# Performance work log

Measured on AMD Instinct MI355X. Metric: run time of the kernel, lower is better.

## Reference

```python
import jax, jax.numpy as jnp
import numpy as np

N_NODES = 100000
N_EDGES = 3200000


def gcn_conv(x, src, dst, W, b, n):
    # PyG GCNConv: add self-loops, symmetric normalization, scatter-add to dst.
    loops = jnp.arange(n)
    s = jnp.concatenate([src, loops])
    d = jnp.concatenate([dst, loops])
    h = x @ W                                   # [N, out]
    deg = jnp.zeros((n,), h.dtype).at[d].add(1.0)
    dinv = jnp.where(deg > 0, jax.lax.rsqrt(deg), 0.0)
    norm = dinv[s] * dinv[d]                    # [E+N]
    msg = h[s] * norm[:, None]                  # gather + scale
    out = jax.ops.segment_sum(msg, d, num_segments=n)
    return out + b


def setup_inputs() -> dict:
    key = jax.random.key(0)
    ks = jax.random.split(key, 10)
    x1 = jax.random.normal(ks[0], (N_NODES, 3), dtype=jnp.float32)
    edge_index1 = jax.random.randint(ks[1], (2, N_EDGES), 0, N_NODES, dtype=jnp.int64 if jax.config.jax_enable_x64 else jnp.int32)
    def lin(k, fi, fo):
        s = 1.0 / np.sqrt(fi)
        kw, kb = jax.random.split(k)
        return (jax.random.uniform(kw, (fi, fo), jnp.float32, -s, s),
                jax.random.uniform(kb, (fo,), jnp.float32, -s, s))
    W11, b11 = lin(ks[2], 3, 32)
    W12, b12 = lin(ks[3], 32, 32)
    W13, b13 = lin(ks[4], 32, 32)
    fc_w, fc_b = lin(ks[5], 32, 1)
    return {"x1": x1, "edge_index1": edge_index1,
            "W11": W11, "b11": b11, "W12": W12, "b12": b12,
            "W13": W13, "b13": b13, "fc_w": fc_w, "fc_b": fc_b}


def reference(x1, edge_index1, W11, b11, W12, b12, W13, b13, fc_w, fc_b):
    n = x1.shape[0]
    src, dst = edge_index1[0], edge_index1[1]
    h = gcn_conv(x1, src, dst, W11, b11, n)
    h = jax.nn.relu(h)
    h = gcn_conv(h, src, dst, W12, b12, n)
    h = jax.nn.relu(h)
    h = gcn_conv(h, src, dst, W13, b13, n)
    h = jax.nn.relu(h)
    return h @ fc_w + fc_b                      # [N, 1]
```

## Files before the change

### kernel.cpp

```cpp
#include <hip/hip_runtime.h>
#include <hip/hip_bf16.h>
#include <hip/hip_fp16.h>


#define RBITS  7
#define RNODES 128
#define SBITS  12
#define SNODES 4096
#define BPS    32
#define SMAX   32
#define CE     4096
#define EPT    16
#define LDSCAP 5632

__global__ void k_init(int S, int capS, int* __restrict__ gcur1) {
    int t = threadIdx.x;
    if (t < S) gcur1[t] = t * capS;
}

__global__ void k_bin1(const int* __restrict__ src, const int* __restrict__ dst, int E, int S,
                       int B, int capB, int* __restrict__ gcur1, int* __restrict__ gcur2,
                       unsigned* __restrict__ binned1) {
    __shared__ int cnt[SMAX * 8];
    __shared__ int repOff[SMAX * 8];
    __shared__ int runS[SMAX];
    int tid = threadIdx.x, rep = tid & 7;
    if (tid == 0)
        for (int q = blockIdx.x; q < B; q += gridDim.x) gcur2[q] = q * capB;
    for (int i = tid; i < SMAX * 8; i += 256) cnt[i] = 0;
    __syncthreads();
    int e0 = blockIdx.x * CE;
    int pk[EPT], rnk[EPT], sup[EPT];
#pragma unroll
    for (int j = 0; j < EPT; j++) {
        int e = e0 + j * 256 + tid;
        if (e < E) {
            int d = __builtin_nontemporal_load(dst + e);
            sup[j] = d >> SBITS;
            pk[j]  = (__builtin_nontemporal_load(src + e) << SBITS) | (d & (SNODES - 1));
            rnk[j] = atomicAdd(&cnt[sup[j] * 8 + rep], 1);
        } else sup[j] = -1;
    }
    __syncthreads();
    if (tid < S) {
        int tot = 0;
#pragma unroll
        for (int r = 0; r < 8; r++) { repOff[tid * 8 + r] = tot; tot += cnt[tid * 8 + r]; }
        runS[tid] = tot ? atomicAdd(&gcur1[tid], tot) : 0;
    }
    __syncthreads();
#pragma unroll
    for (int j = 0; j < EPT; j++)
        if (sup[j] >= 0)
            binned1[runS[sup[j]] + repOff[sup[j] * 8 + rep] + rnk[j]] = (unsigned)pk[j];
}

__global__ void k_bin2(const unsigned* __restrict__ binned1, const int* __restrict__ fillEnd,
                       int S, int capS, int* __restrict__ gcur2, unsigned* __restrict__ binned2) {
    __shared__ int send[SMAX];
    __shared__ int cnt[64 * 4];
    __shared__ int repOff[64 * 4];
    __shared__ int runS[64];
    int tid = threadIdx.x, rep = tid & 3;
    if (tid < S) send[tid] = fillEnd[tid];
    for (int i = tid; i < 64 * 4; i += 256) cnt[i] = 0;
    __syncthreads();
    int i0 = blockIdx.x * CE;
    int s0 = i0 / capS;
    int bnd = (s0 + 1) * capS;
    int Sc = S * capS;
    unsigned pk[EPT];
    int rnk[EPT], rb[EPT];
#pragma unroll
    for (int j = 0; j < EPT; j++) {
        int idx = i0 + j * 256 + tid;
        rb[j] = -1;
        if (idx < Sc) {
            int sp = s0 + (idx >= bnd ? 1 : 0);
            if (idx < send[sp]) {
                unsigned p = __builtin_nontemporal_load(binned1 + idx);
                int relB = ((sp - s0) << 5) | ((p >> RBITS) & (BPS - 1));
                pk[j] = p; rb[j] = relB;
                rnk[j] = atomicAdd(&cnt[relB * 4 + rep], 1);
            }
        }
    }
    __syncthreads();
    if (tid < 64) {
        int tot = 0;
#pragma unroll
        for (int r = 0; r < 4; r++) { repOff[tid * 4 + r] = tot; tot += cnt[tid * 4 + r]; }
        int sp = s0 + (tid >> 5);
        if (tot && sp < S) {
            int gb = sp * BPS + (tid & (BPS - 1));
            runS[tid] = atomicAdd(&gcur2[gb], tot);
        }
    }
    __syncthreads();
#pragma unroll
    for (int j = 0; j < EPT; j++)
        if (rb[j] >= 0) {
            unsigned p = pk[j];
            binned2[runS[rb[j]] + repOff[rb[j] * 4 + rep] + rnk[j]] =
                ((p >> SBITS) << RBITS) | (p & (RNODES - 1));
        }
}

__global__ void k_sortb2(const unsigned* __restrict__ binned2, const int* __restrict__ gcur2,
                         int capB, int N, int* __restrict__ ssort,
                         int2* __restrict__ row2, float* __restrict__ dinv,
                         const float* __restrict__ x, float4* __restrict__ p4) {
    __shared__ int cnt[RNODES];
    __shared__ int cnt2[RNODES];
    __shared__ int loc[RNODES];
    __shared__ int cur2[RNODES];
    __shared__ unsigned sbuf[LDSCAP];
    __shared__ unsigned short rnk16[LDSCAP];
    int b = blockIdx.x, tid = threadIdx.x;
    int beg = b * capB, end = gcur2[b];
    int tot = end - beg;
    int stg = tot < LDSCAP ? tot : LDSCAP;
    if (tid < RNODES) { cnt[tid] = 0; cnt2[tid] = 0; }
    __syncthreads();
    for (int i = tid; i < stg; i += 256) {
        unsigned p = __builtin_nontemporal_load(binned2 + beg + i);
        sbuf[i] = p;
        rnk16[i] = (unsigned short)atomicAdd(&cnt[p & (RNODES - 1)], 1);
    }
    for (int i = LDSCAP + tid; i < tot; i += 256)
        atomicAdd(&cnt2[__builtin_nontemporal_load(binned2 + beg + i) & (RNODES - 1)], 1);
    __syncthreads();
    if (tid < RNODES) loc[tid] = cnt[tid] + cnt2[tid];
    __syncthreads();
    for (int off = 1; off < RNODES; off <<= 1) {
        int v = 0;
        if (tid < RNODES && tid >= off) v = loc[tid - off];
        __syncthreads();
        if (tid < RNODES) loc[tid] += v;
        __syncthreads();
    }
    int n0 = b << RBITS;
    if (tid < RNODES) {
        int ctot = cnt[tid] + cnt2[tid];
        int excl = loc[tid] - ctot;
        loc[tid] = beg + excl;
        cur2[tid] = cnt[tid];
        int n = n0 + tid;
        if (n < N) {
            row2[n] = make_int2(beg + excl, beg + excl + ctot);
            float dv = rsqrtf((float)ctot + 1.0f);
            dinv[n] = dv;
            p4[n] = make_float4(x[n * 3] * dv, x[n * 3 + 1] * dv,
                                x[n * 3 + 2] * dv, 0.f);
        }
    }
    __syncthreads();
    for (int i = tid; i < stg; i += 256) {
        unsigned p = sbuf[i];
        int dl = (int)(p & (RNODES - 1));
        ssort[loc[dl] + rnk16[i]] = (int)(p >> RBITS);
    }
    for (int i = LDSCAP + tid; i < tot; i += 256) {
        unsigned p = __builtin_nontemporal_load(binned2 + beg + i);
        int dl = (int)(p & (RNODES - 1));
        int r  = atomicAdd(&cur2[dl], 1);
        ssort[loc[dl] + r] = (int)(p >> RBITS);
    }
}

__global__ void k_l1g(const int2* __restrict__ row2, const int* __restrict__ ssort,
                      const float4* __restrict__ p4, const float* __restrict__ dinv,
                      const float* __restrict__ W1, const float* __restrict__ b1,
                      const float* __restrict__ W2, __half* __restrict__ g2, int N) {
    __shared__ float sW1[96];
    __shared__ float sb1[32];
    __shared__ float sW2[1024];
    __shared__ float sh1[256];
    int tid = threadIdx.x;
    for (int i = tid; i < 1024; i += 256) sW2[i] = W2[i];
    if (tid < 96) sW1[tid] = W1[tid];
    if (tid < 32) sb1[tid] = b1[tid];
    __syncthreads();
    int t = blockIdx.x * 256 + tid;
    int n = t >> 5, c = t & 31;
    bool active = (n < N);
    float ax = 0.f, ay = 0.f, az = 0.f;
    float di = 0.f;
    float4 me = make_float4(0.f, 0.f, 0.f, 0.f);
    if (active) {
        me = p4[n];
        di = dinv[n];
        int2 r = row2[n];
        for (int idx = r.x + c; idx < r.y; idx += 32) {
            float4 q = p4[__builtin_nontemporal_load(ssort + idx)];
            ax += q.x; ay += q.y; az += q.z;
        }
    }
#pragma unroll
    for (int off = 16; off; off >>= 1) {
        ax += __shfl_xor(ax, off, 32);
        ay += __shfl_xor(ay, off, 32);
        az += __shfl_xor(az, off, 32);
    }
    float h1 = 0.f;
    if (active) {
        ax = di * (ax + me.x); ay = di * (ay + me.y); az = di * (az + me.z);
        h1 = fmaxf(ax * sW1[c] + ay * sW1[32 + c] + az * sW1[64 + c] + sb1[c], 0.f);
    }
    sh1[tid] = h1;
    __syncthreads();
    if (!active) return;
    const float* hr = sh1 + (tid >> 5) * 32;
    float acc = 0.f;
#pragma unroll
    for (int k = 0; k < 32; k++) acc += hr[k] * sW2[k * 32 + c];
    g2[(size_t)n * 32 + c] = __float2half_rn(acc * di);
}

__global__ void __launch_bounds__(256, 8)
k_agg16g(const int2* __restrict__ row2, const int* __restrict__ ssort,
         const __half2* __restrict__ g2, const float* __restrict__ dinv,
         const float* __restrict__ bias, const float* __restrict__ W3,
         __half* __restrict__ gout, int N) {
    __shared__ float sW[1024];
    __shared__ float sh[16 * 33];
    int tid = threadIdx.x;
    for (int i = tid; i < 1024; i += 256) sW[i] = W3[i];
    int t = blockIdx.x * 256 + tid;
    int n = t >> 4, l = t & 15;
    int c0 = l * 2;
    bool act = (n < N);
    float di = 0.f;
    if (act) {
        float2 self = __half22float2(g2[(size_t)n * 16 + l]);
        di = dinv[n];
        int2 r = row2[n];
        int beg = r.x, end = r.y;
        float ax = 0.f, ay = 0.f, bx = 0.f, by = 0.f;
        float cx = 0.f, cy = 0.f, dx = 0.f, dy = 0.f;
        float ex = 0.f, ey = 0.f, fx = 0.f, fy = 0.f;
        float gx = 0.f, gy = 0.f, hx = 0.f, hy = 0.f;
        int base = beg;
        int m = end - base; if (m > 16) m = 16;
        int myS = (m > 0 && l < m) ? __builtin_nontemporal_load(ssort + base + l) : 0;
        while (base < end) {
            int nbase = base + 16;
            int nm = end - nbase; if (nm > 16) nm = 16;
            int nS = (nm > 0 && l < nm) ? __builtin_nontemporal_load(ssort + nbase + l) : 0;
            int i = 0;
            for (; i + 8 <= m; i += 8) {
                int s0 = __shfl(myS, i,     16);
                int s1 = __shfl(myS, i + 1, 16);
                int s2 = __shfl(myS, i + 2, 16);
                int s3 = __shfl(myS, i + 3, 16);
                int s4 = __shfl(myS, i + 4, 16);
                int s5 = __shfl(myS, i + 5, 16);
                int s6 = __shfl(myS, i + 6, 16);
                int s7 = __shfl(myS, i + 7, 16);
                float2 q0 = __half22float2(g2[(size_t)s0 * 16 + l]);
                float2 q1 = __half22float2(g2[(size_t)s1 * 16 + l]);
                float2 q2 = __half22float2(g2[(size_t)s2 * 16 + l]);
                float2 q3 = __half22float2(g2[(size_t)s3 * 16 + l]);
                float2 q4 = __half22float2(g2[(size_t)s4 * 16 + l]);
                float2 q5 = __half22float2(g2[(size_t)s5 * 16 + l]);
                float2 q6 = __half22float2(g2[(size_t)s6 * 16 + l]);
                float2 q7 = __half22float2(g2[(size_t)s7 * 16 + l]);
                ax += q0.x; ay += q0.y;
                bx += q1.x; by += q1.y;
                cx += q2.x; cy += q2.y;
                dx += q3.x; dy += q3.y;
                ex += q4.x; ey += q4.y;
                fx += q5.x; fy += q5.y;
                gx += q6.x; gy += q6.y;
                hx += q7.x; hy += q7.y;
            }
            for (; i + 4 <= m; i += 4) {
                int s0 = __shfl(myS, i,     16);
                int s1 = __shfl(myS, i + 1, 16);
                int s2 = __shfl(myS, i + 2, 16);
                int s3 = __shfl(myS, i + 3, 16);
                float2 q0 = __half22float2(g2[(size_t)s0 * 16 + l]);
                float2 q1 = __half22float2(g2[(size_t)s1 * 16 + l]);
                float2 q2 = __half22float2(g2[(size_t)s2 * 16 + l]);
                float2 q3 = __half22float2(g2[(size_t)s3 * 16 + l]);
                ax += q0.x; ay += q0.y;
                bx += q1.x; by += q1.y;
                cx += q2.x; cy += q2.y;
                dx += q3.x; dy += q3.y;
            }
            for (; i < m; i++) {
                int s = __shfl(myS, i, 16);
                float2 q = __half22float2(g2[(size_t)s * 16 + l]);
                ax += q.x; ay += q.y;
            }
            base = nbase; m = nm; myS = nS;
        }
        float sx = (((ax + bx) + (cx + dx)) + ((ex + fx) + (gx + hx))) + self.x;
        float sy = (((ay + by) + (cy + dy)) + ((ey + fy) + (gy + hy))) + self.y;
        int nn = tid >> 4;
        sh[nn * 33 + c0]     = fmaxf(di * sx + bias[c0], 0.f);
        sh[nn * 33 + c0 + 1] = fmaxf(di * sy + bias[c0 + 1], 0.f);
    }
    __syncthreads();
    if (!act) return;
    const float* hr = sh + (tid >> 4) * 33;
    float a0 = 0.f, a1 = 0.f;
#pragma unroll
    for (int k = 0; k < 32; k++) {
        float hv = hr[k];
        float2 w = *(const float2*)(sW + k * 32 + c0);
        a0 += hv * w.x; a1 += hv * w.y;
    }
    __half2 o = __floats2half2_rn(a0 * di, a1 * di);
    *(__half2*)(gout + (size_t)n * 32 + c0) = o;
}

__global__ void __launch_bounds__(256, 8)
k_agg16_fc(const int2* __restrict__ row2, const int* __restrict__ ssort,
           const __half2* __restrict__ g2, const float* __restrict__ dinv,
           const float* __restrict__ bias, const float* __restrict__ fcw,
           const float* __restrict__ fcb, float* __restrict__ out, int N) {
    int t = blockIdx.x * blockDim.x + threadIdx.x;
    int n = t >> 4, l = t & 15;
    if (n >= N) return;
    float2 self = __half22float2(g2[(size_t)n * 16 + l]);
    float di = dinv[n];
    int2 r = row2[n];
    int beg = r.x, end = r.y;
    float ax = 0.f, ay = 0.f, bx = 0.f, by = 0.f;
    float cx = 0.f, cy = 0.f, dx = 0.f, dy = 0.f;
    float ex = 0.f, ey = 0.f, fx = 0.f, fy = 0.f;
    float gx = 0.f, gy = 0.f, hx = 0.f, hy = 0.f;
    int base = beg;
    int m = end - base; if (m > 16) m = 16;
    int myS = (m > 0 && l < m) ? __builtin_nontemporal_load(ssort + base + l) : 0;
    while (base < end) {
        int nbase = base + 16;
        int nm = end - nbase; if (nm > 16) nm = 16;
        int nS = (nm > 0 && l < nm) ? __builtin_nontemporal_load(ssort + nbase + l) : 0;
        int i = 0;
        for (; i + 8 <= m; i += 8) {
            int s0 = __shfl(myS, i,     16);
            int s1 = __shfl(myS, i + 1, 16);
            int s2 = __shfl(myS, i + 2, 16);
            int s3 = __shfl(myS, i + 3, 16);
            int s4 = __shfl(myS, i + 4, 16);
            int s5 = __shfl(myS, i + 5, 16);
            int s6 = __shfl(myS, i + 6, 16);
            int s7 = __shfl(myS, i + 7, 16);
            float2 q0 = __half22float2(g2[(size_t)s0 * 16 + l]);
            float2 q1 = __half22float2(g2[(size_t)s1 * 16 + l]);
            float2 q2 = __half22float2(g2[(size_t)s2 * 16 + l]);
            float2 q3 = __half22float2(g2[(size_t)s3 * 16 + l]);
            float2 q4 = __half22float2(g2[(size_t)s4 * 16 + l]);
            float2 q5 = __half22float2(g2[(size_t)s5 * 16 + l]);
            float2 q6 = __half22float2(g2[(size_t)s6 * 16 + l]);
            float2 q7 = __half22float2(g2[(size_t)s7 * 16 + l]);
            ax += q0.x; ay += q0.y;
            bx += q1.x; by += q1.y;
            cx += q2.x; cy += q2.y;
            dx += q3.x; dy += q3.y;
            ex += q4.x; ey += q4.y;
            fx += q5.x; fy += q5.y;
            gx += q6.x; gy += q6.y;
            hx += q7.x; hy += q7.y;
        }
        for (; i + 4 <= m; i += 4) {
            int s0 = __shfl(myS, i,     16);
            int s1 = __shfl(myS, i + 1, 16);
            int s2 = __shfl(myS, i + 2, 16);
            int s3 = __shfl(myS, i + 3, 16);
            float2 q0 = __half22float2(g2[(size_t)s0 * 16 + l]);
            float2 q1 = __half22float2(g2[(size_t)s1 * 16 + l]);
            float2 q2 = __half22float2(g2[(size_t)s2 * 16 + l]);
            float2 q3 = __half22float2(g2[(size_t)s3 * 16 + l]);
            ax += q0.x; ay += q0.y;
            bx += q1.x; by += q1.y;
            cx += q2.x; cy += q2.y;
            dx += q3.x; dy += q3.y;
        }
        for (; i < m; i++) {
            int s = __shfl(myS, i, 16);
            float2 q = __half22float2(g2[(size_t)s * 16 + l]);
            ax += q.x; ay += q.y;
        }
        base = nbase; m = nm; myS = nS;
    }
    float sx = (((ax + bx) + (cx + dx)) + ((ex + fx) + (gx + hx))) + self.x;
    float sy = (((ay + by) + (cy + dy)) + ((ey + fy) + (gy + hy))) + self.y;
    int c0 = l * 2;
    float v = fmaxf(di * sx + bias[c0], 0.f) * fcw[c0]
            + fmaxf(di * sy + bias[c0 + 1], 0.f) * fcw[c0 + 1];
    v += __shfl_down(v, 8, 16);
    v += __shfl_down(v, 4, 16);
    v += __shfl_down(v, 2, 16);
    v += __shfl_down(v, 1, 16);
    if (l == 0) out[n] = v + fcb[0];
}

extern "C" void kernel_launch(void* const* d_in, const int* in_sizes, int n_in,
                              void* d_out, int out_size, void* d_ws, size_t ws_size,
                              hipStream_t stream) {
    const float* x1  = (const float*)d_in[0];
    const int*   ei  = (const int*)d_in[1];
    const float* W11 = (const float*)d_in[2];
    const float* b11 = (const float*)d_in[3];
    const float* W12 = (const float*)d_in[4];
    const float* b12 = (const float*)d_in[5];
    const float* W13 = (const float*)d_in[6];
    const float* b13 = (const float*)d_in[7];
    const float* fcw = (const float*)d_in[8];
    const float* fcb = (const float*)d_in[9];
    float* out = (float*)d_out;

    const int N = in_sizes[0] / 3;
    const int E = in_sizes[1] / 2;
    const int* src = ei;
    const int* dst = ei + E;

    const int B = (N + RNODES - 1) / RNODES;
    const int S = (N + SNODES - 1) / SNODES;
    const int capS = E / S + E / S / 16 + 1024;
    const int capB = E / B + E / B / 4 + 256;
    const size_t NC = (size_t)N * 32;

    float4*   p4      = (float4*)d_ws;
    __half*   g       = (__half*)(p4 + N);
    int2*     row2    = (int2*)(g + NC);
    float*    dinv    = (float*)(row2 + N);
    int*      gcur1   = (int*)(dinv + N);
    int*      gcur2   = gcur1 + 32;
    unsigned* binned1 = (unsigned*)(gcur2 + 800);
    unsigned* binned2 = binned1 + (size_t)S * capS;
    int*      ssort   = (int*)(binned2 + (size_t)B * capB);
    __half*   gout    = (__half*)binned1;

    dim3 blk(256);
    dim3 grid_nc(((int)NC + 255) / 256);
    dim3 grid_n16(((N * 16) + 255) / 256);
    dim3 grid_e((E + CE - 1) / CE);
    dim3 grid_sc((S * capS + CE - 1) / CE);
    dim3 grid_b(B);

    k_init<<<dim3(1), blk, 0, stream>>>(S, capS, gcur1);
    k_bin1<<<grid_e, blk, 0, stream>>>(src, dst, E, S, B, capB, gcur1, gcur2, binned1);
    k_bin2<<<grid_sc, blk, 0, stream>>>(binned1, gcur1, S, capS, gcur2, binned2);
    k_sortb2<<<grid_b, blk, 0, stream>>>(binned2, gcur2, capB, N, ssort, row2, dinv, x1, p4);

    k_l1g<<<grid_nc, blk, 0, stream>>>(row2, ssort, p4, dinv, W11, b11, W12, g, N);

    k_agg16g<<<grid_n16, blk, 0, stream>>>(row2, ssort, (const __half2*)g, dinv, b12, W13, gout, N);

    k_agg16_fc<<<grid_n16, blk, 0, stream>>>(row2, ssort, (const __half2*)gout, dinv, b13, fcw, fcb, out, N);
}
```

Measured before the change: 203.1 us.

## Split neighbor gathers into two source-range passes for cache locality

Each node's sorted neighbor list is split by whether the source index falls in the lower or upper half of the node range, and rowq now holds begin/mid/end offsets. Layers 2 and 3 each become two kernels. The first gathers only low-half sources and writes fp32 partial sums to a scratch buffer. The second gathers high-half sources, adds the partial sum, and finishes the layer. The aim is for each pass's random feature gathers to touch about half the feature table, so it fits better in L2/MALL. The cost is two extra launches and an extra write and read of a partial-sum buffer per layer.

```diff
diff --git a/kernel.cpp b/kernel.cpp
--- a/kernel.cpp
+++ b/kernel.cpp
@@ -107,68 +107,75 @@
 }
 
 __global__ void k_sortb2(const unsigned* __restrict__ binned2, const int* __restrict__ gcur2,
-                         int capB, int N, int* __restrict__ ssort,
-                         int2* __restrict__ row2, float* __restrict__ dinv,
+                         int capB, int N, int N2, int* __restrict__ ssort,
+                         int4* __restrict__ rowq, float* __restrict__ dinv,
                          const float* __restrict__ x, float4* __restrict__ p4) {
-    __shared__ int cnt[RNODES];
-    __shared__ int cnt2[RNODES];
-    __shared__ int loc[RNODES];
-    __shared__ int cur2[RNODES];
+    __shared__ int cnt[256];
+    __shared__ int cnt2[256];
+    __shared__ int loc[256];
+    __shared__ int cur2[256];
     __shared__ unsigned sbuf[LDSCAP];
     __shared__ unsigned short rnk16[LDSCAP];
     int b = blockIdx.x, tid = threadIdx.x;
-    int beg = b * capB, end = gcur2[b];
-    int tot = end - beg;
+    int beg0 = b * capB, end = gcur2[b];
+    int tot = end - beg0;
     int stg = tot < LDSCAP ? tot : LDSCAP;
-    if (tid < RNODES) { cnt[tid] = 0; cnt2[tid] = 0; }
+    cnt[tid] = 0; cnt2[tid] = 0;
     __syncthreads();
     for (int i = tid; i < stg; i += 256) {
-        unsigned p = __builtin_nontemporal_load(binned2 + beg + i);
+        unsigned p = __builtin_nontemporal_load(binned2 + beg0 + i);
         sbuf[i] = p;
-        rnk16[i] = (unsigned short)atomicAdd(&cnt[p & (RNODES - 1)], 1);
-    }
-    for (int i = LDSCAP + tid; i < tot; i += 256)
-        atomicAdd(&cnt2[__builtin_nontemporal_load(binned2 + beg + i) & (RNODES - 1)], 1);
-    __syncthreads();
-    if (tid < RNODES) loc[tid] = cnt[tid] + cnt2[tid];
-    __syncthreads();
-    for (int off = 1; off < RNODES; off <<= 1) {
-        int v = 0;
-        if (tid < RNODES && tid >= off) v = loc[tid - off];
+        int bin = (int)((p & (RNODES - 1)) << 1) | ((int)(p >> RBITS) >= N2 ? 1 : 0);
+        rnk16[i] = (unsigned short)atomicAdd(&cnt[bin], 1);
+    }
+    for (int i = LDSCAP + tid; i < tot; i += 256) {
+        unsigned p = __builtin_nontemporal_load(binned2 + beg0 + i);
+        int bin = (int)((p & (RNODES - 1)) << 1) | ((int)(p >> RBITS) >= N2 ? 1 : 0);
+        atomicAdd(&cnt2[bin], 1);
+    }
+    __syncthreads();
+    loc[tid] = cnt[tid] + cnt2[tid];
+    __syncthreads();
+    for (int off = 1; off < 256; off <<= 1) {
+        int v = (tid >= off) ? loc[tid - off] : 0;
         __syncthreads();
-        if (tid < RNODES) loc[tid] += v;
+        loc[tid] += v;
         __syncthreads();
     }
+    int myTot = cnt[tid] + cnt2[tid];
+    int myBase = beg0 + loc[tid] - myTot;
+    __syncthreads();
+    loc[tid] = myBase;
+    cur2[tid] = cnt[tid];
+    __syncthreads();
     int n0 = b << RBITS;
     if (tid < RNODES) {
-        int ctot = cnt[tid] + cnt2[tid];
-        int excl = loc[tid] - ctot;
-        loc[tid] = beg + excl;
-        cur2[tid] = cnt[tid];
+        int begN = loc[2 * tid];
+        int midN = loc[2 * tid + 1];
+        int endN = midN + cnt[2 * tid + 1] + cnt2[2 * tid + 1];
         int n = n0 + tid;
         if (n < N) {
-            row2[n] = make_int2(beg + excl, beg + excl + ctot);
-            float dv = rsqrtf((float)ctot + 1.0f);
+            rowq[n] = make_int4(begN, midN, endN, 0);
+            float dv = rsqrtf((float)(endN - begN) + 1.0f);
             dinv[n] = dv;
             p4[n] = make_float4(x[n * 3] * dv, x[n * 3 + 1] * dv,
                                 x[n * 3 + 2] * dv, 0.f);
         }
     }
-    __syncthreads();
     for (int i = tid; i < stg; i += 256) {
         unsigned p = sbuf[i];
-        int dl = (int)(p & (RNODES - 1));
-        ssort[loc[dl] + rnk16[i]] = (int)(p >> RBITS);
+        int bin = (int)((p & (RNODES - 1)) << 1) | ((int)(p >> RBITS) >= N2 ? 1 : 0);
+        ssort[loc[bin] + rnk16[i]] = (int)(p >> RBITS);
     }
     for (int i = LDSCAP + tid; i < tot; i += 256) {
-        unsigned p = __builtin_nontemporal_load(binned2 + beg + i);
-        int dl = (int)(p & (RNODES - 1));
-        int r  = atomicAdd(&cur2[dl], 1);
-        ssort[loc[dl] + r] = (int)(p >> RBITS);
-    }
-}
-
-__global__ void k_l1g(const int2* __restrict__ row2, const int* __restrict__ ssort,
+        unsigned p = __builtin_nontemporal_load(binned2 + beg0 + i);
+        int bin = (int)((p & (RNODES - 1)) << 1) | ((int)(p >> RBITS) >= N2 ? 1 : 0);
+        int r = atomicAdd(&cur2[bin], 1);
+        ssort[loc[bin] + r] = (int)(p >> RBITS);
+    }
+}
+
+__global__ void k_l1g(const int4* __restrict__ rowq, const int* __restrict__ ssort,
                       const float4* __restrict__ p4, const float* __restrict__ dinv,
                       const float* __restrict__ W1, const float* __restrict__ b1,
                       const float* __restrict__ W2, __half* __restrict__ g2, int N) {
@@ -190,8 +197,8 @@
     if (active) {
         me = p4[n];
         di = dinv[n];
-        int2 r = row2[n];
-        for (int idx = r.x + c; idx < r.y; idx += 32) {
+        int4 r = rowq[n];
+        for (int idx = r.x + c; idx < r.z; idx += 32) {
             float4 q = p4[__builtin_nontemporal_load(ssort + idx)];
             ax += q.x; ay += q.y; az += q.z;
         }
@@ -217,11 +224,83 @@
     g2[(size_t)n * 32 + c] = __float2half_rn(acc * di);
 }
 
+#define GATHER_BODY(base0, lim)                                              \
+    int base = (base0);                                                      \
+    int m = (lim) - base; if (m > 16) m = 16;                                \
+    int myS = (m > 0 && l < m) ? __builtin_nontemporal_load(ssort + base + l) : 0; \
+    while (base < (lim)) {                                                   \
+        int nbase = base + 16;                                               \
+        int nm = (lim) - nbase; if (nm > 16) nm = 16;                        \
+        int nS = (nm > 0 && l < nm) ? __builtin_nontemporal_load(ssort + nbase + l) : 0; \
+        int i = 0;                                                           \
+        for (; i + 8 <= m; i += 8) {                                         \
+            int s0 = __shfl(myS, i,     16);                                 \
+            int s1 = __shfl(myS, i + 1, 16);                                 \
+            int s2 = __shfl(myS, i + 2, 16);                                 \
+            int s3 = __shfl(myS, i + 3, 16);                                 \
+            int s4 = __shfl(myS, i + 4, 16);                                 \
+            int s5 = __shfl(myS, i + 5, 16);                                 \
+            int s6 = __shfl(myS, i + 6, 16);                                 \
+            int s7 = __shfl(myS, i + 7, 16);                                 \
+            float2 q0 = __half22float2(g2[(size_t)s0 * 16 + l]);             \
+            float2 q1 = __half22float2(g2[(size_t)s1 * 16 + l]);             \
+            float2 q2 = __half22float2(g2[(size_t)s2 * 16 + l]);             \
+            float2 q3 = __half22float2(g2[(size_t)s3 * 16 + l]);             \
+            float2 q4 = __half22float2(g2[(size_t)s4 * 16 + l]);             \
+            float2 q5 = __half22float2(g2[(size_t)s5 * 16 + l]);             \
+            float2 q6 = __half22float2(g2[(size_t)s6 * 16 + l]);             \
+            float2 q7 = __half22float2(g2[(size_t)s7 * 16 + l]);             \
+            ax += q0.x; ay += q0.y; bx += q1.x; by += q1.y;                  \
+            cx += q2.x; cy += q2.y; dx += q3.x; dy += q3.y;                  \
+            ex += q4.x; ey += q4.y; fx += q5.x; fy += q5.y;                  \
+            gx += q6.x; gy += q6.y; hx += q7.x; hy += q7.y;                  \
+        }                                                                    \
+        for (; i + 4 <= m; i += 4) {                                         \
+            int s0 = __shfl(myS, i,     16);                                 \
+            int s1 = __shfl(myS, i + 1, 16);                                 \
+            int s2 = __shfl(myS, i + 2, 16);                                 \
+            int s3 = __shfl(myS, i + 3, 16);                                 \
+            float2 q0 = __half22float2(g2[(size_t)s0 * 16 + l]);             \
+            float2 q1 = __half22float2(g2[(size_t)s1 * 16 + l]);             \
+            float2 q2 = __half22float2(g2[(size_t)s2 * 16 + l]);             \
+            float2 q3 = __half22float2(g2[(size_t)s3 * 16 + l]);             \
+            ax += q0.x; ay += q0.y; bx += q1.x; by += q1.y;                  \
+            cx += q2.x; cy += q2.y; dx += q3.x; dy += q3.y;                  \
+        }                                                                    \
+        for (; i < m; i++) {                                                 \
+            int s = __shfl(myS, i, 16);                                      \
+            float2 q = __half22float2(g2[(size_t)s * 16 + l]);               \
+            ax += q.x; ay += q.y;                                            \
+        }                                                                    \
+        base = nbase; m = nm; myS = nS;                                      \
+    }
+
 __global__ void __launch_bounds__(256, 8)
-k_agg16g(const int2* __restrict__ row2, const int* __restrict__ ssort,
-         const __half2* __restrict__ g2, const float* __restrict__ dinv,
-         const float* __restrict__ bias, const float* __restrict__ W3,
-         __half* __restrict__ gout, int N) {
+k_aggA(const int4* __restrict__ rowq, const int* __restrict__ ssort,
+       const __half2* __restrict__ g2, float2* __restrict__ hp, int N, int N2) {
+    int t = blockIdx.x * blockDim.x + threadIdx.x;
+    int n = t >> 4, l = t & 15;
+    if (n >= N) return;
+    float2 self = make_float2(0.f, 0.f);
+    if (n < N2) self = __half22float2(g2[(size_t)n * 16 + l]);
+    int4 r = rowq[n];
+    float ax = 0.f, ay = 0.f, bx = 0.f, by = 0.f;
+    float cx = 0.f, cy = 0.f, dx = 0.f, dy = 0.f;
+    float ex = 0.f, ey = 0.f, fx = 0.f, fy = 0.f;
+    float gx = 0.f, gy = 0.f, hx = 0.f, hy = 0.f;
+    GATHER_BODY(r.x, r.y)
+    float sx = (((ax + bx) + (cx + dx)) + ((ex + fx) + (gx + hx))) + self.x;
+    float sy = (((ay + by) + (cy + dy)) + ((ey + fy) + (gy + hy))) + self.y;
+    float2 o = make_float2(sx, sy);
+    double od; __builtin_memcpy(&od, &o, 8);
+    __builtin_nontemporal_store(od, (double*)(hp + (size_t)n * 16 + l));
+}
+
+__global__ void __launch_bounds__(256, 8)
+k_agg16gB(const int4* __restrict__ rowq, const int* __restrict__ ssort,
+          const __half2* __restrict__ g2, const float2* __restrict__ hp,
+          const float* __restrict__ dinv, const float* __restrict__ bias,
+          const float* __restrict__ W3, __half* __restrict__ gout, int N, int N2) {
     __shared__ float sW[1024];
     __shared__ float sh[16 * 33];
     int tid = threadIdx.x;
@@ -232,71 +311,19 @@
     bool act = (n < N);
     float di = 0.f;
     if (act) {
-        float2 self = __half22float2(g2[(size_t)n * 16 + l]);
+        float2 self = make_float2(0.f, 0.f);
+        if (n >= N2) self = __half22float2(g2[(size_t)n * 16 + l]);
+        double pd = __builtin_nontemporal_load((const double*)(hp + (size_t)n * 16 + l));
+        float2 part; __builtin_memcpy(&part, &pd, 8);
         di = dinv[n];
-        int2 r = row2[n];
-        int beg = r.x, end = r.y;
+        int4 r = rowq[n];
         float ax = 0.f, ay = 0.f, bx = 0.f, by = 0.f;
         float cx = 0.f, cy = 0.f, dx = 0.f, dy = 0.f;
         float ex = 0.f, ey = 0.f, fx = 0.f, fy = 0.f;
         float gx = 0.f, gy = 0.f, hx = 0.f, hy = 0.f;
-        int base = beg;
-        int m = end - base; if (m > 16) m = 16;
-        int myS = (m > 0 && l < m) ? __builtin_nontemporal_load(ssort + base + l) : 0;
-        while (base < end) {
-            int nbase = base + 16;
-            int nm = end - nbase; if (nm > 16) nm = 16;
-            int nS = (nm > 0 && l < nm) ? __builtin_nontemporal_load(ssort + nbase + l) : 0;
-            int i = 0;
-            for (; i + 8 <= m; i += 8) {
-                int s0 = __shfl(myS, i,     16);
-                int s1 = __shfl(myS, i + 1, 16);
-                int s2 = __shfl(myS, i + 2, 16);
-                int s3 = __shfl(myS, i + 3, 16);
-                int s4 = __shfl(myS, i + 4, 16);
-                int s5 = __shfl(myS, i + 5, 16);
-                int s6 = __shfl(myS, i + 6, 16);
-                int s7 = __shfl(myS, i + 7, 16);
-                float2 q0 = __half22float2(g2[(size_t)s0 * 16 + l]);
-                float2 q1 = __half22float2(g2[(size_t)s1 * 16 + l]);
-                float2 q2 = __half22float2(g2[(size_t)s2 * 16 + l]);
-                float2 q3 = __half22float2(g2[(size_t)s3 * 16 + l]);
-                float2 q4 = __half22float2(g2[(size_t)s4 * 16 + l]);
-                float2 q5 = __half22float2(g2[(size_t)s5 * 16 + l]);
-                float2 q6 = __half22float2(g2[(size_t)s6 * 16 + l]);
-                float2 q7 = __half22float2(g2[(size_t)s7 * 16 + l]);
-                ax += q0.x; ay += q0.y;
-                bx += q1.x; by += q1.y;
-                cx += q2.x; cy += q2.y;
-                dx += q3.x; dy += q3.y;
-                ex += q4.x; ey += q4.y;
-                fx += q5.x; fy += q5.y;
-                gx += q6.x; gy += q6.y;
-                hx += q7.x; hy += q7.y;
-            }
-            for (; i + 4 <= m; i += 4) {
-                int s0 = __shfl(myS, i,     16);
-                int s1 = __shfl(myS, i + 1, 16);
-                int s2 = __shfl(myS, i + 2, 16);
-                int s3 = __shfl(myS, i + 3, 16);
-                float2 q0 = __half22float2(g2[(size_t)s0 * 16 + l]);
-                float2 q1 = __half22float2(g2[(size_t)s1 * 16 + l]);
-                float2 q2 = __half22float2(g2[(size_t)s2 * 16 + l]);
-                float2 q3 = __half22float2(g2[(size_t)s3 * 16 + l]);
-                ax += q0.x; ay += q0.y;
-                bx += q1.x; by += q1.y;
-                cx += q2.x; cy += q2.y;
-                dx += q3.x; dy += q3.y;
-            }
-            for (; i < m; i++) {
-                int s = __shfl(myS, i, 16);
-                float2 q = __half22float2(g2[(size_t)s * 16 + l]);
-                ax += q.x; ay += q.y;
-            }
-            base = nbase; m = nm; myS = nS;
-        }
-        float sx = (((ax + bx) + (cx + dx)) + ((ex + fx) + (gx + hx))) + self.x;
-        float sy = (((ay + by) + (cy + dy)) + ((ey + fy) + (gy + hy))) + self.y;
+        GATHER_BODY(r.y, r.z)
+        float sx = (((ax + bx) + (cx + dx)) + ((ex + fx) + (gx + hx))) + self.x + part.x;
+        float sy = (((ay + by) + (cy + dy)) + ((ey + fy) + (gy + hy))) + self.y + part.y;
         int nn = tid >> 4;
         sh[nn * 33 + c0]     = fmaxf(di * sx + bias[c0], 0.f);
         sh[nn * 33 + c0 + 1] = fmaxf(di * sy + bias[c0 + 1], 0.f);
@@ -316,78 +343,27 @@
 }
 
 __global__ void __launch_bounds__(256, 8)
-k_agg16_fc(const int2* __restrict__ row2, const int* __restrict__ ssort,
-           const __half2* __restrict__ g2, const float* __restrict__ dinv,
-           const float* __restrict__ bias, const float* __restrict__ fcw,
-           const float* __restrict__ fcb, float* __restrict__ out, int N) {
+k_aggfcB(const int4* __restrict__ rowq, const int* __restrict__ ssort,
+         const __half2* __restrict__ g2, const float2* __restrict__ hp,
+         const float* __restrict__ dinv, const float* __restrict__ bias,
+         const float* __restrict__ fcw, const float* __restrict__ fcb,
+         float* __restrict__ out, int N, int N2) {
     int t = blockIdx.x * blockDim.x + threadIdx.x;
     int n = t >> 4, l = t & 15;
     if (n >= N) return;
-    float2 self = __half22float2(g2[(size_t)n * 16 + l]);
+    float2 self = make_float2(0.f, 0.f);
+    if (n >= N2) self = __half22float2(g2[(size_t)n * 16 + l]);
+    double pd = __builtin_nontemporal_load((const double*)(hp + (size_t)n * 16 + l));
+    float2 part; __builtin_memcpy(&part, &pd, 8);
     float di = dinv[n];
-    int2 r = row2[n];
-    int beg = r.x, end = r.y;
+    int4 r = rowq[n];
     float ax = 0.f, ay = 0.f, bx = 0.f, by = 0.f;
     float cx = 0.f, cy = 0.f, dx = 0.f, dy = 0.f;
     float ex = 0.f, ey = 0.f, fx = 0.f, fy = 0.f;
     float gx = 0.f, gy = 0.f, hx = 0.f, hy = 0.f;
-    int base = beg;
-    int m = end - base; if (m > 16) m = 16;
-    int myS = (m > 0 && l < m) ? __builtin_nontemporal_load(ssort + base + l) : 0;
-    while (base < end) {
-        int nbase = base + 16;
-        int nm = end - nbase; if (nm > 16) nm = 16;
-        int nS = (nm > 0 && l < nm) ? __builtin_nontemporal_load(ssort + nbase + l) : 0;
-        int i = 0;
-        for (; i + 8 <= m; i += 8) {
-            int s0 = __shfl(myS, i,     16);
-            int s1 = __shfl(myS, i + 1, 16);
-            int s2 = __shfl(myS, i + 2, 16);
-            int s3 = __shfl(myS, i + 3, 16);
-            int s4 = __shfl(myS, i + 4, 16);
-            int s5 = __shfl(myS, i + 5, 16);
-            int s6 = __shfl(myS, i + 6, 16);
-            int s7 = __shfl(myS, i + 7, 16);
-            float2 q0 = __half22float2(g2[(size_t)s0 * 16 + l]);
-            float2 q1 = __half22float2(g2[(size_t)s1 * 16 + l]);
-            float2 q2 = __half22float2(g2[(size_t)s2 * 16 + l]);
-            float2 q3 = __half22float2(g2[(size_t)s3 * 16 + l]);
-            float2 q4 = __half22float2(g2[(size_t)s4 * 16 + l]);
-            float2 q5 = __half22float2(g2[(size_t)s5 * 16 + l]);
-            float2 q6 = __half22float2(g2[(size_t)s6 * 16 + l]);
-            float2 q7 = __half22float2(g2[(size_t)s7 * 16 + l]);
-            ax += q0.x; ay += q0.y;
-            bx += q1.x; by += q1.y;
-            cx += q2.x; cy += q2.y;
-            dx += q3.x; dy += q3.y;
-            ex += q4.x; ey += q4.y;
-            fx += q5.x; fy += q5.y;
-            gx += q6.x; gy += q6.y;
-            hx += q7.x; hy += q7.y;
-        }
-        for (; i + 4 <= m; i += 4) {
-            int s0 = __shfl(myS, i,     16);
-            int s1 = __shfl(myS, i + 1, 16);
-            int s2 = __shfl(myS, i + 2, 16);
-            int s3 = __shfl(myS, i + 3, 16);
-            float2 q0 = __half22float2(g2[(size_t)s0 * 16 + l]);
-            float2 q1 = __half22float2(g2[(size_t)s1 * 16 + l]);
-            float2 q2 = __half22float2(g2[(size_t)s2 * 16 + l]);
-            float2 q3 = __half22float2(g2[(size_t)s3 * 16 + l]);
-            ax += q0.x; ay += q0.y;
-            bx += q1.x; by += q1.y;
-            cx += q2.x; cy += q2.y;
-            dx += q3.x; dy += q3.y;
-        }
-        for (; i < m; i++) {
-            int s = __shfl(myS, i, 16);
-            float2 q = __half22float2(g2[(size_t)s * 16 + l]);
-            ax += q.x; ay += q.y;
-        }
-        base = nbase; m = nm; myS = nS;
-    }
-    float sx = (((ax + bx) + (cx + dx)) + ((ex + fx) + (gx + hx))) + self.x;
-    float sy = (((ay + by) + (cy + dy)) + ((ey + fy) + (gy + hy))) + self.y;
+    GATHER_BODY(r.y, r.z)
+    float sx = (((ax + bx) + (cx + dx)) + ((ex + fx) + (gx + hx))) + self.x + part.x;
+    float sy = (((ay + by) + (cy + dy)) + ((ey + fy) + (gy + hy))) + self.y + part.y;
     int c0 = l * 2;
     float v = fmaxf(di * sx + bias[c0], 0.f) * fcw[c0]
             + fmaxf(di * sy + bias[c0 + 1], 0.f) * fcw[c0 + 1];
@@ -395,7 +371,7 @@
     v += __shfl_down(v, 4, 16);
     v += __shfl_down(v, 2, 16);
     v += __shfl_down(v, 1, 16);
-    if (l == 0) out[n] = v + fcb[0];
+    if (l == 0) __builtin_nontemporal_store(v + fcb[0], out + n);
 }
 
 extern "C" void kernel_launch(void* const* d_in, const int* in_sizes, int n_in,
@@ -415,6 +391,7 @@
 
     const int N = in_sizes[0] / 3;
     const int E = in_sizes[1] / 2;
+    const int N2 = N / 2;
     const int* src = ei;
     const int* dst = ei + E;
 
@@ -426,14 +403,15 @@
 
     float4*   p4      = (float4*)d_ws;
     __half*   g       = (__half*)(p4 + N);
-    int2*     row2    = (int2*)(g + NC);
-    float*    dinv    = (float*)(row2 + N);
+    int4*     rowq    = (int4*)(g + NC);
+    float*    dinv    = (float*)(rowq + N);
     int*      gcur1   = (int*)(dinv + N);
     int*      gcur2   = gcur1 + 32;
     unsigned* binned1 = (unsigned*)(gcur2 + 800);
     unsigned* binned2 = binned1 + (size_t)S * capS;
     int*      ssort   = (int*)(binned2 + (size_t)B * capB);
     __half*   gout    = (__half*)binned1;
+    float2*   hpart   = (float2*)binned2;
 
     dim3 blk(256);
     dim3 grid_nc(((int)NC + 255) / 256);
@@ -445,11 +423,13 @@
     k_init<<<dim3(1), blk, 0, stream>>>(S, capS, gcur1);
     k_bin1<<<grid_e, blk, 0, stream>>>(src, dst, E, S, B, capB, gcur1, gcur2, binned1);
     k_bin2<<<grid_sc, blk, 0, stream>>>(binned1, gcur1, S, capS, gcur2, binned2);
-    k_sortb2<<<grid_b, blk, 0, stream>>>(binned2, gcur2, capB, N, ssort, row2, dinv, x1, p4);
-
-    k_l1g<<<grid_nc, blk, 0, stream>>>(row2, ssort, p4, dinv, W11, b11, W12, g, N);
-
-    k_agg16g<<<grid_n16, blk, 0, stream>>>(row2, ssort, (const __half2*)g, dinv, b12, W13, gout, N);
-
-    k_agg16_fc<<<grid_n16, blk, 0, stream>>>(row2, ssort, (const __half2*)gout, dinv, b13, fcw, fcb, out, N);
-}
+    k_sortb2<<<grid_b, blk, 0, stream>>>(binned2, gcur2, capB, N, N2, ssort, rowq, dinv, x1, p4);
+
+    k_l1g<<<grid_nc, blk, 0, stream>>>(rowq, ssort, p4, dinv, W11, b11, W12, g, N);
+
+    k_aggA<<<grid_n16, blk, 0, stream>>>(rowq, ssort, (const __half2*)g, hpart, N, N2);
+    k_agg16gB<<<grid_n16, blk, 0, stream>>>(rowq, ssort, (const __half2*)g, hpart, dinv, b12, W13, gout, N, N2);
+
+    k_aggA<<<grid_n16, blk, 0, stream>>>(rowq, ssort, (const __half2*)gout, hpart, N, N2);
+    k_aggfcB<<<grid_n16, blk, 0, stream>>>(rowq, ssort, (const __half2*)gout, hpart, dinv, b13, fcw, fcb, out, N, N2);
+}
```

New measurement: 223.6 us. 1.1x slower.
